# Kernel tuning notes

Measured on AMD Instinct MI355X. Metric: run time of the kernel, lower is better.

## Reference

```python
import jax, jax.numpy as jnp
import numpy as np

N_NODES = 50000
N_EDGES = 400000
N_GRAPHS = 64
D_IN = 256
D_HID = 256
D_OUT = 16


def _gcn_conv(x, edge_index, W, b):
    """PyG-style GCNConv: h = D^{-1/2}(A+I)D^{-1/2} (x @ W) + b."""
    n = x.shape[0]
    loop = jnp.arange(n)
    src = jnp.concatenate([edge_index[0], loop])  # [E+N]
    dst = jnp.concatenate([edge_index[1], loop])
    deg = jax.ops.segment_sum(jnp.ones_like(dst, x.dtype), dst, num_segments=n)
    dinv = jnp.where(deg > 0, jax.lax.rsqrt(deg), jnp.zeros_like(deg))
    norm = dinv[src] * dinv[dst]  # [E+N]
    h = x @ W  # linear transform first (as PyG does)
    msg = h[src] * norm[:, None]  # gather + scale, [E+N, D]
    out = jax.ops.segment_sum(msg, dst, num_segments=n)  # scatter-add
    return out + b


def setup_inputs() -> dict:
    key = jax.random.key(0)
    ks = jax.random.split(key, 12)
    x = jax.random.normal(ks[0], (N_NODES, D_IN), dtype=jnp.float32)
    edge_index = jax.random.randint(ks[1], (2, N_EDGES), 0, N_NODES, dtype=jnp.int64)
    batch = jnp.sort(jax.random.randint(ks[2], (N_NODES,), 0, N_GRAPHS, dtype=jnp.int64))

    def glorot(k, fan_in, fan_out):
        s = np.sqrt(6.0 / (fan_in + fan_out)).astype(np.float32)
        return jax.random.uniform(k, (fan_in, fan_out), jnp.float32, -s, s)

    return {
        "x": x,
        "edge_index": edge_index,
        "batch": batch,
        "W1": glorot(ks[3], D_IN, D_HID), "b1": jnp.zeros((D_HID,), jnp.float32),
        "W2": glorot(ks[4], D_HID, D_HID), "b2": jnp.zeros((D_HID,), jnp.float32),
        "W3": glorot(ks[5], D_HID, D_HID), "b3": jnp.zeros((D_HID,), jnp.float32),
        "Wfc": glorot(ks[6], D_HID, D_OUT), "bfc": jnp.zeros((D_OUT,), jnp.float32),
    }


def reference(x, edge_index, batch, W1, b1, W2, b2, W3, b3, Wfc, bfc):
    h = jax.nn.relu(_gcn_conv(x, edge_index, W1, b1))
    h = jax.nn.relu(_gcn_conv(h, edge_index, W2, b2))
    h = jax.nn.relu(_gcn_conv(h, edge_index, W3, b3))
    # global_mean_pool over batch ids
    sums = jax.ops.segment_sum(h, batch, num_segments=N_GRAPHS)  # [G, D]
    cnts = jax.ops.segment_sum(jnp.ones_like(batch, h.dtype), batch, num_segments=N_GRAPHS)
    pooled = sums / jnp.maximum(cnts, 1.0)[:, None]
    return pooled @ Wfc + bfc  # [G, D_OUT]
```

## Files before the change

### kernel.cpp

```cpp
#include <hip/hip_runtime.h>

#define NN 50000
#define NE 400000
#define NG 64
#define D 256
#define DOUT 16

typedef __attribute__((ext_vector_type(8))) short bf16x8;
typedef __attribute__((ext_vector_type(4))) float f32x4;

__device__ __forceinline__ short f2bf(float x) {
    union { float f; unsigned u; } v; v.f = x;
    unsigned r = v.u + 0x7fffu + ((v.u >> 16) & 1u);
    return (short)(r >> 16);
}
__device__ __forceinline__ float bf2f(short h) {
    union { float f; unsigned u; } v;
    v.u = ((unsigned)(unsigned short)h) << 16;
    return v.f;
}

__device__ __forceinline__ void async_cp16(void* lds, const void* g) {
    __builtin_amdgcn_global_load_lds(
        (const __attribute__((address_space(1))) unsigned int*)g,
        (__attribute__((address_space(3))) unsigned int*)lds, 16, 0, 0);
}


__global__ void k_init(int* __restrict__ cnt, float* __restrict__ pooled,
                       const int* __restrict__ batch, float* __restrict__ inv_cnt,
                       int n) {
    int i = blockIdx.x * 256 + threadIdx.x;
    if (i < n) cnt[i] = 0;
    if (i < NG * D) pooled[i] = 0.f;
    if (blockIdx.x == 0 && threadIdx.x < NG) {
        int g = threadIdx.x;
        int lo = 0, hi = n;
        while (lo < hi) { int mid = (lo + hi) >> 1; if (batch[mid] < g) lo = mid + 1; else hi = mid; }
        int start = lo;
        hi = n;
        while (lo < hi) { int mid = (lo + hi) >> 1; if (batch[mid] < g + 1) lo = mid + 1; else hi = mid; }
        inv_cnt[g] = 1.f / fmaxf((float)(lo - start), 1.f);
    }
}

__global__ void k_count(const int* __restrict__ eidx, int* __restrict__ cnt, int E) {
    int e = blockIdx.x * blockDim.x + threadIdx.x;
    if (e < E) atomicAdd(&cnt[eidx[E + e]], 1);
}

__global__ void k_scan1(const int* __restrict__ cnt, int* __restrict__ excl,
                        int* __restrict__ bsums, float* __restrict__ dinv, int n) {
    __shared__ int sh[256];
    int tid = threadIdx.x;
    int base = blockIdx.x * 1024;
    int v[4]; int tsum = 0;
    for (int j = 0; j < 4; ++j) {
        int i = base + tid * 4 + j;
        v[j] = (i < n) ? cnt[i] : 0;
        if (i < n) dinv[i] = rsqrtf((float)(v[j] + 1));
        tsum += v[j];
    }
    sh[tid] = tsum; __syncthreads();
    for (int d = 1; d < 256; d <<= 1) {
        int t = (tid >= d) ? sh[tid - d] : 0;
        __syncthreads();
        sh[tid] += t;
        __syncthreads();
    }
    int run = sh[tid] - tsum;
    for (int j = 0; j < 4; ++j) {
        int i = base + tid * 4 + j;
        if (i < n) excl[i] = run;
        run += v[j];
    }
    if (tid == 255) bsums[blockIdx.x] = sh[255];
}

__global__ void k_scan2(int* bsums, int nb) {
    __shared__ int sh[64];
    int tid = threadIdx.x;
    int v = (tid < nb) ? bsums[tid] : 0;
    sh[tid] = v; __syncthreads();
    for (int d = 1; d < 64; d <<= 1) {
        int t = (tid >= d) ? sh[tid - d] : 0;
        __syncthreads();
        sh[tid] += t;
        __syncthreads();
    }
    if (tid < nb) bsums[tid] = sh[tid] - v;
}

__global__ void k_scan3(int* __restrict__ row_ptr, const int* __restrict__ bsums,
                        int* __restrict__ cursor, int n, int E) {
    int i = blockIdx.x * blockDim.x + threadIdx.x;
    if (i < n) {
        int v = row_ptr[i] + bsums[i >> 10];
        row_ptr[i] = v;
        cursor[i] = v;
    }
    if (i == 0) row_ptr[n] = E;
}

__global__ void k_fill(const int* __restrict__ eidx, int* __restrict__ cursor,
                       int* __restrict__ col_src, int E) {
    int e = blockIdx.x * blockDim.x + threadIdx.x;
    if (e < E) {
        int d = eidx[E + e];
        int pos = atomicAdd(&cursor[d], 1);
        col_src[pos] = eidx[e];
    }
}


__global__ void k_split(const float* __restrict__ x, unsigned short* __restrict__ ahi,
                        int total4, int xblocks,
                        const float* __restrict__ W1, short* __restrict__ w1hi, short* __restrict__ w1lo,
                        const float* __restrict__ W2, short* __restrict__ w2hi, short* __restrict__ w2lo,
                        const float* __restrict__ W3, short* __restrict__ w3hi, short* __restrict__ w3lo) {
    if (blockIdx.x < (unsigned)xblocks) {
        int i = blockIdx.x * 256 + threadIdx.x;
        if (i >= total4) return;
        float4 v = ((const float4*)x)[i];
        ushort4 h;
        h.x = (unsigned short)f2bf(v.x);
        h.y = (unsigned short)f2bf(v.y);
        h.z = (unsigned short)f2bf(v.z);
        h.w = (unsigned short)f2bf(v.w);
        ((ushort4*)ahi)[i] = h;
    } else {
        int wb = blockIdx.x - xblocks;
        int which = wb >> 8;
        int idx = (wb & 255) * 256 + threadIdx.x;
        int nn = idx >> 8, k = idx & 255;
        const float* W = (which == 0) ? W1 : (which == 1) ? W2 : W3;
        short* Whi = (which == 0) ? w1hi : (which == 1) ? w2hi : w3hi;
        short* Wlo = (which == 0) ? w1lo : (which == 1) ? w2lo : w3lo;
        float xv = W[k * 256 + nn];
        short h = f2bf(xv);
        Whi[idx] = h;
        Wlo[idx] = f2bf(xv - bf2f(h));
    }
}


__global__ __launch_bounds__(256, 2) void k_gemm_mfma(
        const unsigned short* __restrict__ A,
        const short* __restrict__ Whi, const short* __restrict__ Wlo,
        const float* __restrict__ dinv, unsigned short* __restrict__ C, int M) {
    __shared__ short Ah_s[8192];
    __shared__ short Bh_s[16384];
    __shared__ short Bl_s[16384];

    const int tid = threadIdx.x;
    const int bm = blockIdx.x * 128;

    const int lane = tid & 63;
    const int w    = tid >> 6;
    const int wm   = w & 1;
    const int wn   = w >> 1;
    const int lm   = lane & 15;
    const int quad = lane >> 4;

    const int srow = tid >> 3, c = tid & 7;
    const int q = c ^ ((srow >> 1) & 7);
    const unsigned short* pa[4];
    #pragma unroll
    for (int j = 0; j < 4; ++j) {
        int ga = bm + j * 32 + srow; if (ga >= M) ga = M - 1;
        pa[j] = A + ((size_t)ga << 8) + q * 8;
    }
    const short* pbh[8]; const short* pbl[8];
    #pragma unroll
    for (int j = 0; j < 8; ++j) {
        pbh[j] = Whi + ((size_t)(j * 32 + srow) << 8) + q * 8;
        pbl[j] = Wlo + ((size_t)(j * 32 + srow) << 8) + q * 8;
    }

    int st[8];
    #pragma unroll
    for (int j = 0; j < 8; ++j) st[j] = j * 2048 + w * 512;

    int oa[4], ob[8];
    #pragma unroll
    for (int i = 0; i < 4; ++i) {
        int ra = wm * 64 + i * 16 + lm;
        oa[i] = ra * 64 + ((quad ^ ((ra >> 1) & 7)) * 8);
    }
    #pragma unroll
    for (int i = 0; i < 8; ++i) {
        int rb = wn * 128 + i * 16 + lm;
        ob[i] = rb * 64 + ((quad ^ ((rb >> 1) & 7)) * 8);
    }

    f32x4 acc[4][8];
    #pragma unroll
    for (int i = 0; i < 4; ++i)
        #pragma unroll
        for (int j = 0; j < 8; ++j)
            acc[i][j] = (f32x4){0.f, 0.f, 0.f, 0.f};

    for (int k0 = 0; k0 < D; k0 += 64) {
        #pragma unroll
        for (int j = 0; j < 4; ++j) async_cp16(&Ah_s[st[j]], pa[j] + k0);
        #pragma unroll
        for (int j = 0; j < 8; ++j) {
            async_cp16(&Bh_s[st[j]], pbh[j] + k0);
            async_cp16(&Bl_s[st[j]], pbl[j] + k0);
        }
        __syncthreads();

        #pragma unroll
        for (int kh = 0; kh < 2; ++kh) {
            const int xo = kh * 32;
            bf16x8 Ah[4], Bh[8], Bl[8];
            #pragma unroll
            for (int i = 0; i < 4; ++i) Ah[i] = *(const bf16x8*)&Ah_s[oa[i] ^ xo];
            #pragma unroll
            for (int i = 0; i < 8; ++i) {
                Bh[i] = *(const bf16x8*)&Bh_s[ob[i] ^ xo];
                Bl[i] = *(const bf16x8*)&Bl_s[ob[i] ^ xo];
            }
            #pragma unroll
            for (int mi = 0; mi < 4; ++mi)
                #pragma unroll
                for (int ni = 0; ni < 8; ++ni) {
                    acc[mi][ni] = __builtin_amdgcn_mfma_f32_16x16x32_bf16(Ah[mi], Bh[ni], acc[mi][ni], 0, 0, 0);
                    acc[mi][ni] = __builtin_amdgcn_mfma_f32_16x16x32_bf16(Ah[mi], Bl[ni], acc[mi][ni], 0, 0, 0);
                }
        }
        __syncthreads();
    }

    #pragma unroll
    for (int mi = 0; mi < 4; ++mi) {
        int rbase = bm + wm * 64 + mi * 16 + quad * 4;
        #pragma unroll
        for (int r = 0; r < 4; ++r) {
            int grow = rbase + r;
            if (grow < M) {
                float s = dinv[grow];
                #pragma unroll
                for (int ni = 0; ni < 8; ++ni) {
                    int col = wn * 128 + ni * 16 + lm;
                    C[(size_t)grow * D + col] = (unsigned short)f2bf(acc[mi][ni][r] * s);
                }
            }
        }
    }
}


__device__ __forceinline__ void agg_two(
        const unsigned short* __restrict__ h, const int* __restrict__ row_ptr,
        const int* __restrict__ col_src, int n0, int n1, bool has1, int lane,
        float4& a0, float4& a1) {
    ushort4 s0 = ((const ushort4*)(h + (size_t)n0 * D))[lane];
    a0 = make_float4(bf2f(s0.x), bf2f(s0.y), bf2f(s0.z), bf2f(s0.w));
    a1 = make_float4(0.f, 0.f, 0.f, 0.f);
    if (has1) {
        ushort4 s1 = ((const ushort4*)(h + (size_t)n1 * D))[lane];
        a1 = make_float4(bf2f(s1.x), bf2f(s1.y), bf2f(s1.z), bf2f(s1.w));
    }
    int c0 = row_ptr[n0], e0 = row_ptr[n0 + 1];
    int c1 = e0, e1 = has1 ? row_ptr[n1 + 1] : e0;

    while (c0 < e0 || c1 < e1) {
        int cnt0 = min(64, e0 - c0); if (cnt0 < 0) cnt0 = 0;
        int cnt1 = min(64, e1 - c1); if (cnt1 < 0) cnt1 = 0;
        int i0 = (lane < cnt0) ? col_src[c0 + lane] : 0;
        int i1 = (lane < cnt1) ? col_src[c1 + lane] : 0;
        int m = max(cnt0, cnt1);
        for (int e = 0; e < m; e += 8) {
            int k0 = cnt0 - e;
            int k1 = cnt1 - e;
            ushort4 u0[8], u1[8];
            #pragma unroll
            for (int j = 0; j < 8; ++j)
                if (j < k0) {
                    int s = __shfl(i0, e + j);
                    u0[j] = ((const ushort4*)(h + (size_t)s * D))[lane];
                }
            #pragma unroll
            for (int j = 0; j < 8; ++j)
                if (j < k1) {
                    int s = __shfl(i1, e + j);
                    u1[j] = ((const ushort4*)(h + (size_t)s * D))[lane];
                }
            #pragma unroll
            for (int j = 0; j < 8; ++j)
                if (j < k0) {
                    a0.x += bf2f(u0[j].x); a0.y += bf2f(u0[j].y);
                    a0.z += bf2f(u0[j].z); a0.w += bf2f(u0[j].w);
                }
            #pragma unroll
            for (int j = 0; j < 8; ++j)
                if (j < k1) {
                    a1.x += bf2f(u1[j].x); a1.y += bf2f(u1[j].y);
                    a1.z += bf2f(u1[j].z); a1.w += bf2f(u1[j].w);
                }
        }
        c0 += cnt0; c1 += cnt1;
    }
}

__global__ __launch_bounds__(256) void k_agg(
        const unsigned short* __restrict__ h, const float* __restrict__ dinv,
        const int* __restrict__ row_ptr, const int* __restrict__ col_src,
        const float* __restrict__ bias,
        unsigned short* __restrict__ ohi, int n) {
    int w = threadIdx.x >> 6, lane = threadIdx.x & 63;
    int n0 = blockIdx.x * 8 + w * 2;
    if (n0 >= n) return;
    int n1 = n0 + 1;
    bool has1 = n1 < n;
    float4 a0, a1;
    agg_two(h, row_ptr, col_src, n0, n1, has1, lane, a0, a1);

    float di0 = dinv[n0];
    float4 b = ((const float4*)bias)[lane];
    ushort4 o0;
    o0.x = (unsigned short)f2bf(fmaxf(a0.x * di0 + b.x, 0.f));
    o0.y = (unsigned short)f2bf(fmaxf(a0.y * di0 + b.y, 0.f));
    o0.z = (unsigned short)f2bf(fmaxf(a0.z * di0 + b.z, 0.f));
    o0.w = (unsigned short)f2bf(fmaxf(a0.w * di0 + b.w, 0.f));
    ((ushort4*)(ohi + (size_t)n0 * D))[lane] = o0;
    if (has1) {
        float di1 = dinv[n1];
        ushort4 o1;
        o1.x = (unsigned short)f2bf(fmaxf(a1.x * di1 + b.x, 0.f));
        o1.y = (unsigned short)f2bf(fmaxf(a1.y * di1 + b.y, 0.f));
        o1.z = (unsigned short)f2bf(fmaxf(a1.z * di1 + b.z, 0.f));
        o1.w = (unsigned short)f2bf(fmaxf(a1.w * di1 + b.w, 0.f));
        ((ushort4*)(ohi + (size_t)n1 * D))[lane] = o1;
    }
}


__global__ __launch_bounds__(256) void k_pool_sum(
        const unsigned short* __restrict__ hi,
        const int* __restrict__ batch, float* __restrict__ pooled, int n) {
    int beg = blockIdx.x * 64;
    if (beg >= n) return;
    int end = min(beg + 64, n);
    int t = threadIdx.x;
    float acc = 0.f;
    int cur = batch[beg];
    for (int i = beg; i < end; ++i) {
        int g = batch[i];
        if (g != cur) {
            atomicAdd(&pooled[cur * D + t], acc);
            acc = 0.f;
            cur = g;
        }
        acc += bf2f(hi[(size_t)i * D + t]);
    }
    atomicAdd(&pooled[cur * D + t], acc);
}


__global__ void k_fc(const float* __restrict__ pooled, const float* __restrict__ inv_cnt,
                     const float* __restrict__ W, const float* __restrict__ b,
                     float* __restrict__ out) {
    int t = blockIdx.x * blockDim.x + threadIdx.x;
    if (t >= NG * DOUT) return;
    int g = t >> 4, o = t & 15;
    float acc = 0.f;
    for (int k = 0; k < D; ++k) acc += pooled[g * D + k] * W[k * DOUT + o];
    out[t] = acc * inv_cnt[g] + b[o];
}


extern "C" void kernel_launch(void* const* d_in, const int* in_sizes, int n_in,
                              void* d_out, int out_size, void* d_ws, size_t ws_size,
                              hipStream_t stream) {
    const float* x    = (const float*)d_in[0];
    const int*   eidx = (const int*)d_in[1];
    const int*   batch= (const int*)d_in[2];
    const float* W1   = (const float*)d_in[3];
    const float* b1   = (const float*)d_in[4];
    const float* W2   = (const float*)d_in[5];
    const float* b2   = (const float*)d_in[6];
    const float* W3   = (const float*)d_in[7];
    const float* b3   = (const float*)d_in[8];
    const float* Wfc  = (const float*)d_in[9];
    const float* bfc  = (const float*)d_in[10];
    float* out = (float*)d_out;

    const int n = in_sizes[0] / D;
    const int E = in_sizes[1] / 2;

    char* p = (char*)d_ws;
    auto take = [&](size_t bytes) -> void* {
        void* q = (void*)p;
        p += (bytes + 255) & ~(size_t)255;
        return q;
    };
    int*   cnt     = (int*)take((size_t)n * 4);
    int*   row_ptr = (int*)take((size_t)(n + 1) * 4);
    int*   cursor  = (int*)take((size_t)n * 4);
    int*   col_src = (int*)take((size_t)E * 4);
    int*   bsums   = (int*)take(256 * 4);
    float* dinv    = (float*)take((size_t)n * 4);
    float* inv_cnt = (float*)take((size_t)NG * 4);
    short* w1hi    = (short*)take((size_t)D * D * 2);
    short* w1lo    = (short*)take((size_t)D * D * 2);
    short* w2hi    = (short*)take((size_t)D * D * 2);
    short* w2lo    = (short*)take((size_t)D * D * 2);
    short* w3hi    = (short*)take((size_t)D * D * 2);
    short* w3lo    = (short*)take((size_t)D * D * 2);
    unsigned short* hbuf = (unsigned short*)take((size_t)n * D * 2);
    unsigned short* ahi  = (unsigned short*)take((size_t)n * D * 2);
    float* pooled  = (float*)take((size_t)NG * D * 4);

    int tb = 256;
    int gn = (n + tb - 1) / tb;
    int ge = (E + tb - 1) / tb;
    int nb = (n + 1023) / 1024;
    int total4 = n * D / 4;
    int xblocks = (total4 + 255) / 256;

    k_init<<<gn, tb, 0, stream>>>(cnt, pooled, batch, inv_cnt, n);
    k_split<<<xblocks + 3 * 256, tb, 0, stream>>>(x, ahi, total4, xblocks,
                                                  W1, w1hi, w1lo, W2, w2hi, w2lo, W3, w3hi, w3lo);
    k_count<<<ge, tb, 0, stream>>>(eidx, cnt, E);
    k_scan1<<<nb, 256, 0, stream>>>(cnt, row_ptr, bsums, dinv, n);
    k_scan2<<<1, 64, 0, stream>>>(bsums, nb);
    k_scan3<<<gn, tb, 0, stream>>>(row_ptr, bsums, cursor, n, E);
    k_fill<<<ge, tb, 0, stream>>>(eidx, cursor, col_src, E);

    int ggrid = (n + 127) / 128;
    int agrid = (n + 7) / 8;

    k_gemm_mfma<<<ggrid, 256, 0, stream>>>(ahi, w1hi, w1lo, dinv, hbuf, n);
    k_agg<<<agrid, 256, 0, stream>>>(hbuf, dinv, row_ptr, col_src, b1, ahi, n);

    k_gemm_mfma<<<ggrid, 256, 0, stream>>>(ahi, w2hi, w2lo, dinv, hbuf, n);
    k_agg<<<agrid, 256, 0, stream>>>(hbuf, dinv, row_ptr, col_src, b2, ahi, n);

    k_gemm_mfma<<<ggrid, 256, 0, stream>>>(ahi, w3hi, w3lo, dinv, hbuf, n);
    k_agg<<<agrid, 256, 0, stream>>>(hbuf, dinv, row_ptr, col_src, b3, ahi, n);

    k_pool_sum<<<(n + 63) / 64, 256, 0, stream>>>(ahi, batch, pooled, n);
    k_fc<<<4, 256, 0, stream>>>(pooled, inv_cnt, Wfc, bfc, out);
}
```

Baseline: 393.6 us.

## Widen aggregation loads to 16 bytes, one node per wave, fuse setup kernels

```diff
diff --git a/kernel.cpp b/kernel.cpp
--- a/kernel.cpp
+++ b/kernel.cpp
@@ -7,6 +7,7 @@
 #define DOUT 16
 
 typedef __attribute__((ext_vector_type(8))) short bf16x8;
+typedef __attribute__((ext_vector_type(8))) unsigned short u16x8;
 typedef __attribute__((ext_vector_type(4))) float f32x4;
 
 __device__ __forceinline__ short f2bf(float x) {
@@ -44,9 +45,40 @@
     }
 }
 
-__global__ void k_count(const int* __restrict__ eidx, int* __restrict__ cnt, int E) {
-    int e = blockIdx.x * blockDim.x + threadIdx.x;
-    if (e < E) atomicAdd(&cnt[eidx[E + e]], 1);
+
+__global__ void k_split_count(const float* __restrict__ x, unsigned short* __restrict__ ahi,
+                              int total4, int xblocks,
+                              const float* __restrict__ W1, short* __restrict__ w1hi, short* __restrict__ w1lo,
+                              const float* __restrict__ W2, short* __restrict__ w2hi, short* __restrict__ w2lo,
+                              const float* __restrict__ W3, short* __restrict__ w3hi, short* __restrict__ w3lo,
+                              const int* __restrict__ eidx, int* __restrict__ cnt, int E) {
+    int b = blockIdx.x;
+    if (b < xblocks) {
+        int i = b * 256 + threadIdx.x;
+        if (i >= total4) return;
+        float4 v = ((const float4*)x)[i];
+        ushort4 h;
+        h.x = (unsigned short)f2bf(v.x);
+        h.y = (unsigned short)f2bf(v.y);
+        h.z = (unsigned short)f2bf(v.z);
+        h.w = (unsigned short)f2bf(v.w);
+        ((ushort4*)ahi)[i] = h;
+    } else if (b < xblocks + 3 * 256) {
+        int wb = b - xblocks;
+        int which = wb >> 8;
+        int idx = (wb & 255) * 256 + threadIdx.x;
+        int nn = idx >> 8, k = idx & 255;
+        const float* W = (which == 0) ? W1 : (which == 1) ? W2 : W3;
+        short* Whi = (which == 0) ? w1hi : (which == 1) ? w2hi : w3hi;
+        short* Wlo = (which == 0) ? w1lo : (which == 1) ? w2lo : w3lo;
+        float xv = W[k * 256 + nn];
+        short h = f2bf(xv);
+        Whi[idx] = h;
+        Wlo[idx] = f2bf(xv - bf2f(h));
+    } else {
+        int e = (b - xblocks - 3 * 256) * 256 + threadIdx.x;
+        if (e < E) atomicAdd(&cnt[eidx[E + e]], 1);
+    }
 }
 
 __global__ void k_scan1(const int* __restrict__ cnt, int* __restrict__ excl,
@@ -77,25 +109,21 @@
     if (tid == 255) bsums[blockIdx.x] = sh[255];
 }
 
-__global__ void k_scan2(int* bsums, int nb) {
-    __shared__ int sh[64];
-    int tid = threadIdx.x;
-    int v = (tid < nb) ? bsums[tid] : 0;
-    sh[tid] = v; __syncthreads();
-    for (int d = 1; d < 64; d <<= 1) {
-        int t = (tid >= d) ? sh[tid - d] : 0;
-        __syncthreads();
-        sh[tid] += t;
-        __syncthreads();
-    }
-    if (tid < nb) bsums[tid] = sh[tid] - v;
-}
-
 __global__ void k_scan3(int* __restrict__ row_ptr, const int* __restrict__ bsums,
-                        int* __restrict__ cursor, int n, int E) {
-    int i = blockIdx.x * blockDim.x + threadIdx.x;
+                        int* __restrict__ cursor, int n, int E, int nb) {
+    __shared__ int off_s;
+    int chunk = (int)(blockIdx.x >> 2);
+    if (threadIdx.x < 64) {
+        int v = ((int)threadIdx.x < nb && (int)threadIdx.x < chunk) ? bsums[threadIdx.x] : 0;
+        #pragma unroll
+        for (int d = 1; d < 64; d <<= 1) v += __shfl_xor(v, d);
+        if (threadIdx.x == 0) off_s = v;
+    }
+    __syncthreads();
+    int off = off_s;
+    int i = blockIdx.x * 256 + threadIdx.x;
     if (i < n) {
-        int v = row_ptr[i] + bsums[i >> 10];
+        int v = row_ptr[i] + off;
         row_ptr[i] = v;
         cursor[i] = v;
     }
@@ -109,37 +137,6 @@
         int d = eidx[E + e];
         int pos = atomicAdd(&cursor[d], 1);
         col_src[pos] = eidx[e];
-    }
-}
-
-
-__global__ void k_split(const float* __restrict__ x, unsigned short* __restrict__ ahi,
-                        int total4, int xblocks,
-                        const float* __restrict__ W1, short* __restrict__ w1hi, short* __restrict__ w1lo,
-                        const float* __restrict__ W2, short* __restrict__ w2hi, short* __restrict__ w2lo,
-                        const float* __restrict__ W3, short* __restrict__ w3hi, short* __restrict__ w3lo) {
-    if (blockIdx.x < (unsigned)xblocks) {
-        int i = blockIdx.x * 256 + threadIdx.x;
-        if (i >= total4) return;
-        float4 v = ((const float4*)x)[i];
-        ushort4 h;
-        h.x = (unsigned short)f2bf(v.x);
-        h.y = (unsigned short)f2bf(v.y);
-        h.z = (unsigned short)f2bf(v.z);
-        h.w = (unsigned short)f2bf(v.w);
-        ((ushort4*)ahi)[i] = h;
-    } else {
-        int wb = blockIdx.x - xblocks;
-        int which = wb >> 8;
-        int idx = (wb & 255) * 256 + threadIdx.x;
-        int nn = idx >> 8, k = idx & 255;
-        const float* W = (which == 0) ? W1 : (which == 1) ? W2 : W3;
-        short* Whi = (which == 0) ? w1hi : (which == 1) ? w2hi : w3hi;
-        short* Wlo = (which == 0) ? w1lo : (which == 1) ? w2lo : w3lo;
-        float xv = W[k * 256 + nn];
-        short h = f2bf(xv);
-        Whi[idx] = h;
-        Wlo[idx] = f2bf(xv - bf2f(h));
     }
 }
 
@@ -251,88 +248,62 @@
 }
 
 
-__device__ __forceinline__ void agg_two(
-        const unsigned short* __restrict__ h, const int* __restrict__ row_ptr,
-        const int* __restrict__ col_src, int n0, int n1, bool has1, int lane,
-        float4& a0, float4& a1) {
-    ushort4 s0 = ((const ushort4*)(h + (size_t)n0 * D))[lane];
-    a0 = make_float4(bf2f(s0.x), bf2f(s0.y), bf2f(s0.z), bf2f(s0.w));
-    a1 = make_float4(0.f, 0.f, 0.f, 0.f);
-    if (has1) {
-        ushort4 s1 = ((const ushort4*)(h + (size_t)n1 * D))[lane];
-        a1 = make_float4(bf2f(s1.x), bf2f(s1.y), bf2f(s1.z), bf2f(s1.w));
-    }
-    int c0 = row_ptr[n0], e0 = row_ptr[n0 + 1];
-    int c1 = e0, e1 = has1 ? row_ptr[n1 + 1] : e0;
-
-    while (c0 < e0 || c1 < e1) {
-        int cnt0 = min(64, e0 - c0); if (cnt0 < 0) cnt0 = 0;
-        int cnt1 = min(64, e1 - c1); if (cnt1 < 0) cnt1 = 0;
-        int i0 = (lane < cnt0) ? col_src[c0 + lane] : 0;
-        int i1 = (lane < cnt1) ? col_src[c1 + lane] : 0;
-        int m = max(cnt0, cnt1);
-        for (int e = 0; e < m; e += 8) {
-            int k0 = cnt0 - e;
-            int k1 = cnt1 - e;
-            ushort4 u0[8], u1[8];
-            #pragma unroll
-            for (int j = 0; j < 8; ++j)
-                if (j < k0) {
-                    int s = __shfl(i0, e + j);
-                    u0[j] = ((const ushort4*)(h + (size_t)s * D))[lane];
-                }
-            #pragma unroll
-            for (int j = 0; j < 8; ++j)
-                if (j < k1) {
-                    int s = __shfl(i1, e + j);
-                    u1[j] = ((const ushort4*)(h + (size_t)s * D))[lane];
-                }
-            #pragma unroll
-            for (int j = 0; j < 8; ++j)
-                if (j < k0) {
-                    a0.x += bf2f(u0[j].x); a0.y += bf2f(u0[j].y);
-                    a0.z += bf2f(u0[j].z); a0.w += bf2f(u0[j].w);
-                }
-            #pragma unroll
-            for (int j = 0; j < 8; ++j)
-                if (j < k1) {
-                    a1.x += bf2f(u1[j].x); a1.y += bf2f(u1[j].y);
-                    a1.z += bf2f(u1[j].z); a1.w += bf2f(u1[j].w);
-                }
-        }
-        c0 += cnt0; c1 += cnt1;
-    }
-}
-
 __global__ __launch_bounds__(256) void k_agg(
         const unsigned short* __restrict__ h, const float* __restrict__ dinv,
         const int* __restrict__ row_ptr, const int* __restrict__ col_src,
         const float* __restrict__ bias,
         unsigned short* __restrict__ ohi, int n) {
     int w = threadIdx.x >> 6, lane = threadIdx.x & 63;
-    int n0 = blockIdx.x * 8 + w * 2;
-    if (n0 >= n) return;
-    int n1 = n0 + 1;
-    bool has1 = n1 < n;
-    float4 a0, a1;
-    agg_two(h, row_ptr, col_src, n0, n1, has1, lane, a0, a1);
-
-    float di0 = dinv[n0];
-    float4 b = ((const float4*)bias)[lane];
-    ushort4 o0;
-    o0.x = (unsigned short)f2bf(fmaxf(a0.x * di0 + b.x, 0.f));
-    o0.y = (unsigned short)f2bf(fmaxf(a0.y * di0 + b.y, 0.f));
-    o0.z = (unsigned short)f2bf(fmaxf(a0.z * di0 + b.z, 0.f));
-    o0.w = (unsigned short)f2bf(fmaxf(a0.w * di0 + b.w, 0.f));
-    ((ushort4*)(ohi + (size_t)n0 * D))[lane] = o0;
-    if (has1) {
-        float di1 = dinv[n1];
-        ushort4 o1;
-        o1.x = (unsigned short)f2bf(fmaxf(a1.x * di1 + b.x, 0.f));
-        o1.y = (unsigned short)f2bf(fmaxf(a1.y * di1 + b.y, 0.f));
-        o1.z = (unsigned short)f2bf(fmaxf(a1.z * di1 + b.z, 0.f));
-        o1.w = (unsigned short)f2bf(fmaxf(a1.w * di1 + b.w, 0.f));
-        ((ushort4*)(ohi + (size_t)n1 * D))[lane] = o1;
+    int node = blockIdx.x * 4 + w;
+    if (node >= n) return;
+    int half = lane >> 5;
+    int dcol = lane & 31;
+
+    float acc[8] = {0.f, 0.f, 0.f, 0.f, 0.f, 0.f, 0.f, 0.f};
+    if (half == 0) {
+        u16x8 sv = ((const u16x8*)(h + (size_t)node * D))[dcol];
+        #pragma unroll
+        for (int d = 0; d < 8; ++d) acc[d] = bf2f((short)sv[d]);
+    }
+
+    int beg = row_ptr[node], end = row_ptr[node + 1];
+    for (int c = beg; c < end; c += 64) {
+        int cnt = min(64, end - c);
+        int myidx = (lane < cnt) ? col_src[c + lane] : 0;
+        for (int e = 0; e < cnt; e += 16) {
+            u16x8 u[8];
+            bool val[8];
+            #pragma unroll
+            for (int j = 0; j < 8; ++j) {
+                int eid = e + j * 2 + half;
+                val[j] = eid < cnt;
+                if (val[j]) {
+                    int s = __shfl(myidx, eid);
+                    u[j] = ((const u16x8*)(h + (size_t)s * D))[dcol];
+                }
+            }
+            #pragma unroll
+            for (int j = 0; j < 8; ++j)
+                if (val[j]) {
+                    #pragma unroll
+                    for (int d = 0; d < 8; ++d) acc[d] += bf2f((short)u[j][d]);
+                }
+        }
+    }
+
+    #pragma unroll
+    for (int d = 0; d < 8; ++d) acc[d] += __shfl_xor(acc[d], 32);
+
+    if (half == 0) {
+        float di = dinv[node];
+        float4 b0 = ((const float4*)bias)[dcol * 2];
+        float4 b1 = ((const float4*)bias)[dcol * 2 + 1];
+        float bb[8] = {b0.x, b0.y, b0.z, b0.w, b1.x, b1.y, b1.z, b1.w};
+        u16x8 o;
+        #pragma unroll
+        for (int d = 0; d < 8; ++d)
+            o[d] = (unsigned short)f2bf(fmaxf(acc[d] * di + bb[d], 0.f));
+        ((u16x8*)(ohi + (size_t)node * D))[dcol] = o;
     }
 }
 
@@ -421,16 +392,16 @@
     int xblocks = (total4 + 255) / 256;
 
     k_init<<<gn, tb, 0, stream>>>(cnt, pooled, batch, inv_cnt, n);
-    k_split<<<xblocks + 3 * 256, tb, 0, stream>>>(x, ahi, total4, xblocks,
-                                                  W1, w1hi, w1lo, W2, w2hi, w2lo, W3, w3hi, w3lo);
-    k_count<<<ge, tb, 0, stream>>>(eidx, cnt, E);
+    k_split_count<<<xblocks + 3 * 256 + ge, tb, 0, stream>>>(
+        x, ahi, total4, xblocks,
+        W1, w1hi, w1lo, W2, w2hi, w2lo, W3, w3hi, w3lo,
+        eidx, cnt, E);
     k_scan1<<<nb, 256, 0, stream>>>(cnt, row_ptr, bsums, dinv, n);
-    k_scan2<<<1, 64, 0, stream>>>(bsums, nb);
-    k_scan3<<<gn, tb, 0, stream>>>(row_ptr, bsums, cursor, n, E);
+    k_scan3<<<gn, tb, 0, stream>>>(row_ptr, bsums, cursor, n, E, nb);
     k_fill<<<ge, tb, 0, stream>>>(eidx, cursor, col_src, E);
 
     int ggrid = (n + 127) / 128;
-    int agrid = (n + 7) / 8;
+    int agrid = (n + 3) / 4;
 
     k_gemm_mfma<<<ggrid, 256, 0, stream>>>(ahi, w1hi, w1lo, dinv, hbuf, n);
     k_agg<<<agrid, 256, 0, stream>>>(hbuf, dinv, row_ptr, col_src, b1, ahi, n);
```

Result: faster. 367.8 us (-6.6%).
